# Performance work log

Hardware: AMD Instinct MI355X
Metric: run time of the kernel (lower is better)

Reference implementation:

```python
import jax, jax.numpy as jnp
import numpy as np

N_NODES = 100000
N_EDGES = 3200000
NEG_SLOPE = 0.2  # PyG GATConv default
EPS = 1e-16      # PyG softmax denominator guard


def setup_inputs() -> dict:
    key = jax.random.key(0)
    ks = jax.random.split(key, 12)
    x = jax.random.normal(ks[0], (N_NODES, 4), dtype=jnp.float32)
    edge_index = jax.random.randint(ks[1], (2, N_EDGES), 0, N_NODES, dtype=jnp.int32)
    # conv1: in=4, heads=4, out=16, concat -> 64
    W1 = jax.random.normal(ks[2], (4, 64), dtype=jnp.float32) * 0.5
    a_src1 = jax.random.normal(ks[3], (4, 16), dtype=jnp.float32) * 0.3
    a_dst1 = jax.random.normal(ks[4], (4, 16), dtype=jnp.float32) * 0.3
    b1 = jnp.zeros((64,), dtype=jnp.float32)
    # conv2: in=64, heads=1, out=2, no concat
    W2 = jax.random.normal(ks[5], (64, 2), dtype=jnp.float32) * 0.2
    a_src2 = jax.random.normal(ks[6], (1, 2), dtype=jnp.float32) * 0.3
    a_dst2 = jax.random.normal(ks[7], (1, 2), dtype=jnp.float32) * 0.3
    b2 = jnp.zeros((2,), dtype=jnp.float32)
    return dict(x=x, edge_index=edge_index, W1=W1, a_src1=a_src1, a_dst1=a_dst1,
                b1=b1, W2=W2, a_src2=a_src2, a_dst2=a_dst2, b2=b2)


def _gat_layer(h_in, src, dst, W, a_s, a_d, b, heads, out_dim, concat):
    n = h_in.shape[0]
    h = (h_in @ W).reshape(n, heads, out_dim)            # [N, H, F]
    alpha_s = jnp.einsum('nhf,hf->nh', h, a_s)           # [N, H]
    alpha_d = jnp.einsum('nhf,hf->nh', h, a_d)
    e = jax.nn.leaky_relu(alpha_s[src] + alpha_d[dst], NEG_SLOPE)  # [E, H]
    # segment softmax over incoming edges of each dst node
    m = jax.ops.segment_max(e, dst, num_segments=n)      # [N, H]
    e = jnp.exp(e - m[dst])
    s = jax.ops.segment_sum(e, dst, num_segments=n)
    alpha = e / (s[dst] + EPS)                            # [E, H]
    msg = h[src] * alpha[:, :, None]                      # [E, H, F]
    out = jax.ops.segment_sum(msg, dst, num_segments=n)   # [N, H, F]
    if concat:
        out = out.reshape(n, heads * out_dim)
    else:
        out = out.mean(axis=1)
    return out + b


def reference(x, edge_index, W1, a_src1, a_dst1, b1, W2, a_src2, a_dst2, b2):
    n = x.shape[0]
    loop = jnp.arange(n, dtype=edge_index.dtype)
    src = jnp.concatenate([edge_index[0], loop])  # PyG add_self_loops=True
    dst = jnp.concatenate([edge_index[1], loop])
    h = jax.nn.elu(_gat_layer(x, src, dst, W1, a_src1, a_dst1, b1, 4, 16, True))
    h = _gat_layer(h, src, dst, W2, a_src2, a_dst2, b2, 1, 2, False)
    return jax.nn.log_softmax(h, axis=1)
```

## Files before the change

### kernel.cpp

```cpp
#include <hip/hip_runtime.h>
#include <hip/hip_fp16.h>
#include <math.h>

#define NEG_SLOPE 0.2f
#define EPS_F 1e-16f

#define P1_NB 256
#define P1S_THREADS 1024
#define MAX_BEDGES 10240
#define SCAN_SHIFT 11

__device__ __forceinline__ float leaky(float v) {
    return v >= 0.f ? v : NEG_SLOPE * v;
}

__global__ void k_phaseA(const float* __restrict__ x, const float* __restrict__ W1,
                         const float* __restrict__ a_src1, const float* __restrict__ a_dst1,
                         __half* __restrict__ h1h, float* __restrict__ as1,
                         float* __restrict__ ad1, int N) {
    int node = blockIdx.x * 4 + (threadIdx.x >> 6);
    if (node >= N) return;
    int lane = threadIdx.x & 63;
    float x0 = x[node * 4 + 0], x1 = x[node * 4 + 1];
    float x2 = x[node * 4 + 2], x3 = x[node * 4 + 3];
    float h = x0 * W1[lane] + x1 * W1[64 + lane] + x2 * W1[128 + lane] + x3 * W1[192 + lane];
    h1h[(size_t)node * 64 + lane] = __float2half(h);
    float as = h * a_src1[lane];
    float ad = h * a_dst1[lane];
#pragma unroll
    for (int m = 8; m >= 1; m >>= 1) {
        as += __shfl_xor(as, m, 16);
        ad += __shfl_xor(ad, m, 16);
    }
    if ((lane & 15) == 0) {
        int head = lane >> 4;
        as1[node * 4 + head] = as;
        ad1[node * 4 + head] = ad;
    }
}

__global__ void k_p1hist(const int* __restrict__ dst, int* __restrict__ histT,
                         int E, int chunk, int nbucket) {
    __shared__ int cnt[512];
    int blk = blockIdx.x, t = threadIdx.x;
    for (int i = t; i < nbucket; i += P1S_THREADS) cnt[i] = 0;
    __syncthreads();
    int s = blk * chunk, e = min(E, s + chunk);
    for (int i = s + t; i < e; i += P1S_THREADS)
        atomicAdd(&cnt[dst[i] >> 8], 1);
    __syncthreads();
    for (int i = t; i < nbucket; i += P1S_THREADS)
        histT[i * P1_NB + blk] = cnt[i];
}

__global__ void k_scan1(const int* __restrict__ in, int* __restrict__ out,
                        int* __restrict__ blockSums, int M) {
    __shared__ int sdata[256];
    int t = threadIdx.x;
    int base = blockIdx.x * 2048 + t * 8;
    int v[8];
    int total = 0;
#pragma unroll
    for (int k = 0; k < 8; ++k) {
        int idx = base + k;
        v[k] = (idx < M) ? in[idx] : 0;
        total += v[k];
    }
    sdata[t] = total;
    __syncthreads();
    for (int off = 1; off < 256; off <<= 1) {
        int x = (t >= off) ? sdata[t - off] : 0;
        __syncthreads();
        sdata[t] += x;
        __syncthreads();
    }
    int run = sdata[t] - total;
#pragma unroll
    for (int k = 0; k < 8; ++k) {
        int idx = base + k;
        if (idx < M) out[idx] = run;
        run += v[k];
    }
    if (t == 255) blockSums[blockIdx.x] = sdata[255];
}

__global__ void k_p1scatter(const int* __restrict__ src, const int* __restrict__ dst,
                            const int* __restrict__ baseT, const int* __restrict__ blockSums,
                            int nbScan, unsigned int* __restrict__ packed,
                            int E, int chunk, int nbucket) {
    __shared__ int cnt[512];
    __shared__ int pre[64];
    int blk = blockIdx.x, t = threadIdx.x;
    if (t == 0) {
        int run = 0;
        for (int j = 0; j < nbScan; ++j) { pre[j] = run; run += blockSums[j]; }
    }
    __syncthreads();
    for (int i = t; i < nbucket; i += P1S_THREADS) {
        int idx = i * P1_NB + blk;
        cnt[i] = baseT[idx] + pre[idx >> SCAN_SHIFT];
    }
    __syncthreads();
    int s = blk * chunk, e = min(E, s + chunk);
    for (int i = s + t; i < e; i += P1S_THREADS) {
        int d = dst[i];
        int pos = atomicAdd(&cnt[d >> 8], 1);
        packed[pos] = ((unsigned int)(d & 255) << 23) | (unsigned int)src[i];
    }
}

__global__ void k_fineL1(const unsigned int* __restrict__ packed, const int* __restrict__ baseT,
                         const int* __restrict__ blockSums, int nbScan,
                         const __half* __restrict__ h1h, const float* __restrict__ as1,
                         const float* __restrict__ ad1, const float* __restrict__ b1,
                         const float* __restrict__ W2, const float* __restrict__ a_src2,
                         const float* __restrict__ a_dst2,
                         int* __restrict__ csr, int* __restrict__ rowptr,
                         uint2* __restrict__ node2, int N, int E) {
    __shared__ int cnt[256];
    __shared__ int off[256];
    __shared__ int cur[256];
    __shared__ int sePre[2];
    __shared__ unsigned int eb[MAX_BEDGES];

    int b = blockIdx.x, t = threadIdx.x;
    int nbucket = gridDim.x;
    if (t == 0) {
        int idx0 = b * P1_NB, idx1 = (b + 1) * P1_NB;
        int sb0 = idx0 >> SCAN_SHIFT, sb1 = idx1 >> SCAN_SHIFT;
        int run = 0, p0 = 0, p1 = 0;
        for (int j = 0; j < nbScan; ++j) {
            if (j == sb0) p0 = run;
            if (j == sb1) p1 = run;
            run += blockSums[j];
        }
        sePre[0] = p0; sePre[1] = p1;
    }
    if (t < 256) cnt[t] = 0;
    __syncthreads();
    int startE = baseT[b * P1_NB] + sePre[0];
    int endE = E;
    if (b != nbucket - 1) endE = baseT[(b + 1) * P1_NB] + sePre[1];
    int ne = endE - startE;
    if (ne > MAX_BEDGES) ne = MAX_BEDGES;

    for (int i = t; i < ne; i += 1024)
        atomicAdd(&cnt[packed[startE + i] >> 23], 1);
    __syncthreads();
    if (t < 256) cur[t] = cnt[t];
    __syncthreads();
    for (int o = 1; o < 256; o <<= 1) {
        int v = (t < 256 && t >= o) ? cur[t - o] : 0;
        __syncthreads();
        if (t < 256) cur[t] += v;
        __syncthreads();
    }
    if (t < 256) {
        int excl = cur[t] - cnt[t];
        off[t] = excl;
        int node = (b << 8) + t;
        if (node < N) rowptr[node] = startE + excl;
    }
    if (b == 0 && t == 0) rowptr[N] = E;
    __syncthreads();
    if (t < 256) cur[t] = off[t];
    __syncthreads();
    for (int i = t; i < ne; i += 1024) {
        unsigned int p = packed[startE + i];
        int pos = atomicAdd(&cur[p >> 23], 1);
        eb[pos] = p;
    }
    __syncthreads();
    for (int i = t; i < ne; i += 1024)
        csr[startE + i] = (int)(eb[i] & 0x7FFFFFu);

    int wave = t >> 6;
    int lane = t & 63;
    int head4 = lane & 3;
    int j     = lane >> 2;
    int sub   = lane >> 4;
    int fl    = lane & 15;
    int h     = fl >> 2;
    int nodeBase = b << 8;

    for (int q = 0; q < 16; ++q) {
        int local = wave * 16 + q;
        int node = nodeBase + local;
        if (node >= N) break;
        int beg = off[local];
        int end = beg + cnt[local];

        float ad_s1 = ad1[node * 4 + head4];
        float pself4 = __expf(leaky(as1[node * 4 + head4] + ad_s1));
        float psum = (lane < 4) ? pself4 : 0.f;

        float pselfF = __shfl(pself4, h);
        float a0 = 0.f, a1 = 0.f, a2 = 0.f, a3 = 0.f;
        if (sub == 0) {
            float2 raw = *(const float2*)(h1h + ((size_t)node << 6) + (fl << 2));
            __half2 h01 = *reinterpret_cast<__half2*>(&raw.x);
            __half2 h23 = *reinterpret_cast<__half2*>(&raw.y);
            float2 f01 = __half22float2(h01), f23 = __half22float2(h23);
            a0 = pselfF * f01.x; a1 = pselfF * f01.y;
            a2 = pselfF * f23.x; a3 = pselfF * f23.y;
        }

        for (int c = beg; c < end; c += 16) {
            int e = c + j;
            bool valid = e < end;
            int s = (int)(eb[valid ? e : beg] & 0x7FFFFFu);
            float v = leaky(as1[s * 4 + head4] + ad_s1);
            float p = valid ? __expf(v) : 0.f;
            psum += p;

            int s_q[4];
#pragma unroll
            for (int m = 0; m < 4; ++m) s_q[m] = __shfl(s, m * 16 + sub * 4);
            float2 raw[4];
#pragma unroll
            for (int m = 0; m < 4; ++m)
                raw[m] = *(const float2*)(h1h + ((size_t)s_q[m] << 6) + (fl << 2));
            float p_q[4];
#pragma unroll
            for (int m = 0; m < 4; ++m) p_q[m] = __shfl(p, m * 16 + sub * 4 + h);
#pragma unroll
            for (int m = 0; m < 4; ++m) {
                __half2 h01 = *reinterpret_cast<__half2*>(&raw[m].x);
                __half2 h23 = *reinterpret_cast<__half2*>(&raw[m].y);
                float2 f01 = __half22float2(h01), f23 = __half22float2(h23);
                a0 = fmaf(p_q[m], f01.x, a0);
                a1 = fmaf(p_q[m], f01.y, a1);
                a2 = fmaf(p_q[m], f23.x, a2);
                a3 = fmaf(p_q[m], f23.y, a3);
            }
        }

        a0 += __shfl_xor(a0, 16); a0 += __shfl_xor(a0, 32);
        a1 += __shfl_xor(a1, 16); a1 += __shfl_xor(a1, 32);
        a2 += __shfl_xor(a2, 16); a2 += __shfl_xor(a2, 32);
        a3 += __shfl_xor(a3, 16); a3 += __shfl_xor(a3, 32);

#pragma unroll
        for (int m = 4; m <= 32; m <<= 1) psum += __shfl_xor(psum, m);
        float psumF = __shfl(psum, h);
        float inv = 1.f / (psumF + EPS_F);

        float4 b1v = ((const float4*)b1)[fl];
        float o0 = a0 * inv + b1v.x;
        float o1 = a1 * inv + b1v.y;
        float o2 = a2 * inv + b1v.z;
        float o3 = a3 * inv + b1v.w;
        float e0 = o0 > 0.f ? o0 : (__expf(o0) - 1.f);
        float e1 = o1 > 0.f ? o1 : (__expf(o1) - 1.f);
        float e2 = o2 > 0.f ? o2 : (__expf(o2) - 1.f);
        float e3 = o3 > 0.f ? o3 : (__expf(o3) - 1.f);

        float4 w01 = ((const float4*)W2)[fl * 2];
        float4 w23 = ((const float4*)W2)[fl * 2 + 1];
        float c0 = e0 * w01.x + e1 * w01.z + e2 * w23.x + e3 * w23.z;
        float c1 = e0 * w01.y + e1 * w01.w + e2 * w23.y + e3 * w23.w;
#pragma unroll
        for (int m = 8; m >= 1; m >>= 1) {
            c0 += __shfl_xor(c0, m);
            c1 += __shfl_xor(c1, m);
        }
        if (lane == 0) {
            float as2 = c0 * a_src2[0] + c1 * a_src2[1];
            float ad2 = c0 * a_dst2[0] + c1 * a_dst2[1];
            __half2 hc = __floats2half2_rn(c0, c1);
            __half2 ha = __floats2half2_rn(as2, ad2);
            node2[node] = make_uint2(*(unsigned int*)&hc, *(unsigned int*)&ha);
        }
    }
}

__global__ void k_layer2(const int* __restrict__ rowptr, const int* __restrict__ csr,
                         const uint2* __restrict__ node2, const float* __restrict__ b2,
                         float* __restrict__ out, int N) {
    int node = blockIdx.x * 16 + (threadIdx.x >> 4);
    if (node >= N) return;
    int sl = threadIdx.x & 15;

    uint2 mraw = node2[node];
    __half2 mch = *reinterpret_cast<__half2*>(&mraw.x);
    __half2 mah = *reinterpret_cast<__half2*>(&mraw.y);
    float2 mc = __half22float2(mch);
    float2 ma = __half22float2(mah);
    float ad = ma.y;
    int beg = rowptr[node], end = rowptr[node + 1];

    float psum = 0.f, a0 = 0.f, a1 = 0.f;
    for (int e = beg + sl; e < end; e += 16) {
        uint2 sraw = node2[csr[e]];
        __half2 sch = *reinterpret_cast<__half2*>(&sraw.x);
        __half2 sah = *reinterpret_cast<__half2*>(&sraw.y);
        float2 sc = __half22float2(sch);
        float2 sa = __half22float2(sah);
        float p = __expf(leaky(sa.x + ad));
        psum += p;
        a0 = fmaf(p, sc.x, a0);
        a1 = fmaf(p, sc.y, a1);
    }
    if (sl == 0) {
        float p = __expf(leaky(ma.x + ad));
        psum += p;
        a0 = fmaf(p, mc.x, a0);
        a1 = fmaf(p, mc.y, a1);
    }
#pragma unroll
    for (int m = 8; m >= 1; m >>= 1) {
        psum += __shfl_xor(psum, m);
        a0 += __shfl_xor(a0, m);
        a1 += __shfl_xor(a1, m);
    }
    if (sl == 0) {
        float inv = 1.f / (psum + EPS_F);
        float o0 = a0 * inv + b2[0];
        float o1 = a1 * inv + b2[1];
        float mx = fmaxf(o0, o1);
        float lse = mx + logf(__expf(o0 - mx) + __expf(o1 - mx));
        out[node * 2 + 0] = o0 - lse;
        out[node * 2 + 1] = o1 - lse;
    }
}


extern "C" void kernel_launch(void* const* d_in, const int* in_sizes, int n_in,
                              void* d_out, int out_size, void* d_ws, size_t ws_size,
                              hipStream_t stream) {
    const float* x      = (const float*)d_in[0];
    const int*   ei     = (const int*)d_in[1];
    const float* W1     = (const float*)d_in[2];
    const float* a_src1 = (const float*)d_in[3];
    const float* a_dst1 = (const float*)d_in[4];
    const float* b1     = (const float*)d_in[5];
    const float* W2     = (const float*)d_in[6];
    const float* a_src2 = (const float*)d_in[7];
    const float* a_dst2 = (const float*)d_in[8];
    const float* b2     = (const float*)d_in[9];
    float* out = (float*)d_out;

    int N = in_sizes[0] / 4;
    int E = in_sizes[1] / 2;
    const int* e_src = ei;
    const int* e_dst = ei + E;

    int nbucket = (N + 255) >> 8;
    int M = nbucket * P1_NB;

    char* w = (char*)d_ws;
    auto alloc = [&](size_t bytes) -> void* {
        void* p = (void*)w;
        w += (bytes + 255) & ~(size_t)255;
        return p;
    };
    __half* h1h       = (__half*)alloc((size_t)N * 64 * 2);
    float*  as1       = (float*)alloc((size_t)N * 4 * 4);
    float*  ad1       = (float*)alloc((size_t)N * 4 * 4);
    uint2*  node2     = (uint2*)alloc((size_t)N * 8);
    int*    rowptr    = (int*)alloc((size_t)(N + 1) * 4);
    int*    histT     = (int*)alloc((size_t)M * 4);
    int*    baseT     = (int*)alloc((size_t)M * 4);
    int*    blockSums = (int*)alloc(256 * 4);
    int*    csr       = (int*)alloc((size_t)E * 4);
    unsigned int* packed = (unsigned int*)alloc((size_t)E * 4);

    int chunk = (E + P1_NB - 1) / P1_NB;
    int nbScan = (M + 2047) / 2048;
    int nodeb = (N + 3) / 4;

    k_phaseA<<<nodeb, 256, 0, stream>>>(x, W1, a_src1, a_dst1, h1h, as1, ad1, N);
    k_p1hist<<<P1_NB, P1S_THREADS, 0, stream>>>(e_dst, histT, E, chunk, nbucket);
    k_scan1<<<nbScan, 256, 0, stream>>>(histT, baseT, blockSums, M);
    k_p1scatter<<<P1_NB, P1S_THREADS, 0, stream>>>(e_src, e_dst, baseT, blockSums, nbScan,
                                                   packed, E, chunk, nbucket);
    k_fineL1<<<nbucket, 1024, 0, stream>>>(packed, baseT, blockSums, nbScan,
                                           h1h, as1, ad1, b1, W2,
                                           a_src2, a_dst2, csr, rowptr, node2, N, E);
    k_layer2<<<(N + 15) / 16, 256, 0, stream>>>(rowptr, csr, node2, b2, out, N);
}
```

Measured before the change: 244.1 us.

## Software-pipeline edge gathers in layer-1 aggregation and layer-2 loop

```diff
diff --git a/kernel.cpp b/kernel.cpp
--- a/kernel.cpp
+++ b/kernel.cpp
@@ -170,6 +170,7 @@
         int pos = atomicAdd(&cur[p >> 23], 1);
         eb[pos] = p;
     }
+    if (t == 0 && ne == 0) eb[0] = 0;
     __syncthreads();
     for (int i = t; i < ne; i += 1024)
         csr[startE + i] = (int)(eb[i] & 0x7FFFFFu);
@@ -183,6 +184,38 @@
     int h     = fl >> 2;
     int nodeBase = b << 8;
 
+    auto prefetchChunk = [&](int cb, int ce, bool& pv, float& pasv, float2* praw) {
+        int e = cb + j;
+        bool valid = e < ce;
+        int idx = valid ? e : 0;
+        int s = (int)(eb[idx] & 0x7FFFFFu);
+        pv = valid;
+        pasv = as1[s * 4 + head4];
+        int s_q[4];
+#pragma unroll
+        for (int m = 0; m < 4; ++m) s_q[m] = __shfl(s, m * 16 + sub * 4);
+#pragma unroll
+        for (int m = 0; m < 4; ++m)
+            praw[m] = *(const float2*)(h1h + ((size_t)s_q[m] << 6) + (fl << 2));
+    };
+    auto prefetchNode = [&](int node, float& pad, float& pas, float2& pself) {
+        pad = ad1[node * 4 + head4];
+        pas = as1[node * 4 + head4];
+        pself = *(const float2*)(h1h + ((size_t)node << 6) + (fl << 2));
+    };
+
+    bool vC; float asvC; float2 rawC[4];
+    float adC, asC; float2 hselfC;
+    {
+        int l0 = wave * 16;
+        int n0 = nodeBase + l0;
+        int nn = (n0 < N) ? n0 : nodeBase;
+        prefetchNode(nn, adC, asC, hselfC);
+        int bg = off[l0], en = bg + cnt[l0];
+        if (n0 >= N) { bg = 0; en = 0; }
+        prefetchChunk(bg, en, vC, asvC, rawC);
+    }
+
     for (int q = 0; q < 16; ++q) {
         int local = wave * 16 + q;
         int node = nodeBase + local;
@@ -190,50 +223,64 @@
         int beg = off[local];
         int end = beg + cnt[local];
 
-        float ad_s1 = ad1[node * 4 + head4];
-        float pself4 = __expf(leaky(as1[node * 4 + head4] + ad_s1));
+        float ad_s1 = adC;
+        float pself4 = __expf(leaky(asC + ad_s1));
         float psum = (lane < 4) ? pself4 : 0.f;
-
         float pselfF = __shfl(pself4, h);
         float a0 = 0.f, a1 = 0.f, a2 = 0.f, a3 = 0.f;
         if (sub == 0) {
-            float2 raw = *(const float2*)(h1h + ((size_t)node << 6) + (fl << 2));
-            __half2 h01 = *reinterpret_cast<__half2*>(&raw.x);
-            __half2 h23 = *reinterpret_cast<__half2*>(&raw.y);
+            __half2 h01 = *reinterpret_cast<__half2*>(&hselfC.x);
+            __half2 h23 = *reinterpret_cast<__half2*>(&hselfC.y);
             float2 f01 = __half22float2(h01), f23 = __half22float2(h23);
             a0 = pselfF * f01.x; a1 = pselfF * f01.y;
             a2 = pselfF * f23.x; a3 = pselfF * f23.y;
         }
 
-        for (int c = beg; c < end; c += 16) {
-            int e = c + j;
-            bool valid = e < end;
-            int s = (int)(eb[valid ? e : beg] & 0x7FFFFFu);
-            float v = leaky(as1[s * 4 + head4] + ad_s1);
-            float p = valid ? __expf(v) : 0.f;
-            psum += p;
-
-            int s_q[4];
-#pragma unroll
-            for (int m = 0; m < 4; ++m) s_q[m] = __shfl(s, m * 16 + sub * 4);
-            float2 raw[4];
-#pragma unroll
-            for (int m = 0; m < 4; ++m)
-                raw[m] = *(const float2*)(h1h + ((size_t)s_q[m] << 6) + (fl << 2));
-            float p_q[4];
-#pragma unroll
-            for (int m = 0; m < 4; ++m) p_q[m] = __shfl(p, m * 16 + sub * 4 + h);
-#pragma unroll
-            for (int m = 0; m < 4; ++m) {
-                __half2 h01 = *reinterpret_cast<__half2*>(&raw[m].x);
-                __half2 h23 = *reinterpret_cast<__half2*>(&raw[m].y);
-                float2 f01 = __half22float2(h01), f23 = __half22float2(h23);
-                a0 = fmaf(p_q[m], f01.x, a0);
-                a1 = fmaf(p_q[m], f01.y, a1);
-                a2 = fmaf(p_q[m], f23.x, a2);
-                a3 = fmaf(p_q[m], f23.y, a3);
+        int localN = local + 1;
+        bool hasN = (q < 15) && (nodeBase + localN < N);
+        int nodeN = hasN ? (nodeBase + localN) : node;
+        int begN = hasN ? off[localN] : 0;
+        int endN = hasN ? (begN + cnt[localN]) : 0;
+
+        bool vN; float asvN; float2 rawN[4];
+        float adN, asN; float2 hselfN;
+
+        if (beg >= end) {
+            prefetchNode(nodeN, adN, asN, hselfN);
+            prefetchChunk(begN, endN, vN, asvN, rawN);
+            vC = vN; asvC = asvN;
+#pragma unroll
+            for (int m = 0; m < 4; ++m) rawC[m] = rawN[m];
+        } else {
+            for (int c = beg; c < end; c += 16) {
+                int cn = c + 16;
+                if (cn < end) {
+                    prefetchChunk(cn, end, vN, asvN, rawN);
+                } else {
+                    prefetchNode(nodeN, adN, asN, hselfN);
+                    prefetchChunk(begN, endN, vN, asvN, rawN);
+                }
+                float p = vC ? __expf(leaky(asvC + ad_s1)) : 0.f;
+                psum += p;
+                float p_q[4];
+#pragma unroll
+                for (int m = 0; m < 4; ++m) p_q[m] = __shfl(p, m * 16 + sub * 4 + h);
+#pragma unroll
+                for (int m = 0; m < 4; ++m) {
+                    __half2 h01 = *reinterpret_cast<__half2*>(&rawC[m].x);
+                    __half2 h23 = *reinterpret_cast<__half2*>(&rawC[m].y);
+                    float2 f01 = __half22float2(h01), f23 = __half22float2(h23);
+                    a0 = fmaf(p_q[m], f01.x, a0);
+                    a1 = fmaf(p_q[m], f01.y, a1);
+                    a2 = fmaf(p_q[m], f23.x, a2);
+                    a3 = fmaf(p_q[m], f23.y, a3);
+                }
+                vC = vN; asvC = asvN;
+#pragma unroll
+                for (int m = 0; m < 4; ++m) rawC[m] = rawN[m];
             }
         }
+        adC = adN; asC = asN; hselfC = hselfN;
 
         a0 += __shfl_xor(a0, 16); a0 += __shfl_xor(a0, 32);
         a1 += __shfl_xor(a1, 16); a1 += __shfl_xor(a1, 32);
@@ -290,8 +337,11 @@
     int beg = rowptr[node], end = rowptr[node + 1];
 
     float psum = 0.f, a0 = 0.f, a1 = 0.f;
-    for (int e = beg + sl; e < end; e += 16) {
-        uint2 sraw = node2[csr[e]];
+    int e0 = beg + sl;
+    uint2 sraw = node2[csr[(e0 < end) ? e0 : 0]];
+    for (int e = e0; e < end; e += 16) {
+        int en = e + 16;
+        uint2 snext = node2[csr[(en < end) ? en : 0]];
         __half2 sch = *reinterpret_cast<__half2*>(&sraw.x);
         __half2 sah = *reinterpret_cast<__half2*>(&sraw.y);
         float2 sc = __half22float2(sch);
@@ -300,6 +350,7 @@
         psum += p;
         a0 = fmaf(p, sc.x, a0);
         a1 = fmaf(p, sc.y, a1);
+        sraw = snext;
     }
     if (sl == 0) {
         float p = __expf(leaky(ma.x + ad));
```

New measurement: 263.0 us. 1.08x slower.
